# Optimization experiments

Measured on AMD Instinct MI355X. Metric: run time of the kernel, lower is better.

The kernel has to match this reference:

```python
import jax, jax.numpy as jnp
import numpy as np

EPS = 1e-8  # EPSILON in original repo (sharpen denom); cosine eps matches torch default 1e-8
MAX_SHIFT = 1
M_FEAT = 128


def _lstm_cell(x, h, c, W_ih, W_hh, b_ih, b_hh):
    gates = x @ W_ih.T + b_ih + h @ W_hh.T + b_hh
    i, f, g, o = jnp.split(gates, 4, axis=1)
    c_new = jax.nn.sigmoid(f) * c + jax.nn.sigmoid(i) * jnp.tanh(g)
    h_new = jax.nn.sigmoid(o) * jnp.tanh(c_new)
    return h_new, c_new


def _content_address(bank, k, b):
    # torch cosine_similarity over dim 2: dot / max(|m||k|, eps)
    dot = jnp.einsum('bnm,bm->bn', bank, k)
    denom = jnp.maximum(jnp.linalg.norm(bank, axis=2) * jnp.linalg.norm(k, axis=1, keepdims=True), 1e-8)
    return jax.nn.softmax(b * dot / denom, axis=1)


def _shift(w, s):
    # circular unroll then valid cross-correlation with per-batch kernel s [B, 2*MAX_SHIFT+1]
    wp = jnp.concatenate([w[:, -MAX_SHIFT:], w, w[:, :MAX_SHIFT]], axis=1)
    N = w.shape[1]
    taps = 2 * MAX_SHIFT + 1
    return sum(s[:, i:i + 1] * wp[:, i:i + N] for i in range(taps))


def _sharpen(w, r):
    wr = w ** r
    return wr / (wr.sum(axis=1, keepdims=True) + EPS)


def _move(bank, w_prev, k, b, g, s, r):
    w = _content_address(bank, k, b)
    w = w + (1.0 - g) * w_prev  # faithful: w_c is NOT scaled by g in the source
    w = _shift(w, s)
    return _sharpen(w, r)


def _split_read(p):
    M = M_FEAT
    k = p[:, :M]
    b = jax.nn.softplus(p[:, M:M + 1])
    g = jax.nn.sigmoid(p[:, M + 1:M + 2])
    s = jax.nn.softmax(p[:, M + 2:M + 5], axis=1)
    r = 1.0 + jax.nn.softplus(p[:, M + 5:M + 6])
    return k, b, g, s, r


def _split_write(p):
    M = M_FEAT
    k, b, g, s, r = _split_read(p[:, :M + 6])
    e = jax.nn.sigmoid(p[:, M + 6:M + 6 + M])
    a = p[:, M + 6 + M:M + 6 + 2 * M]
    return k, b, g, s, r, e, a


def setup_inputs() -> dict:
    key = jax.random.key(0)
    ks = jax.random.split(key, 16)
    B, E, H, N, M, O = 64, 256, 512, 4096, 128, 256
    rd_out, wr_out = M + 2 * MAX_SHIFT + 4, 3 * M + 2 * MAX_SHIFT + 4
    sc = 0.05
    return {
        'x': jax.random.normal(ks[0], (B, E), jnp.float32),
        'h_prev': jax.random.normal(ks[1], (B, H), jnp.float32),
        'c_prev': jax.random.normal(ks[2], (B, H), jnp.float32),
        'bank': jax.random.normal(ks[3], (B, N, M), jnp.float32) * 0.1,
        'read_w_prev': jnp.zeros((3, B, N), jnp.float32),
        'write_w_prev': jnp.zeros((3, B, N), jnp.float32),
        'W_ih': jax.random.normal(ks[4], (4 * H, E), jnp.float32) * sc,
        'W_hh': jax.random.normal(ks[5], (4 * H, H), jnp.float32) * sc,
        'b_ih': jax.random.normal(ks[6], (4 * H,), jnp.float32) * sc,
        'b_hh': jax.random.normal(ks[7], (4 * H,), jnp.float32) * sc,
        'read_W': jax.random.normal(ks[8], (3, rd_out, H), jnp.float32) * sc,
        'read_b': jax.random.normal(ks[9], (3, rd_out), jnp.float32) * sc,
        'write_W': jax.random.normal(ks[10], (3, wr_out, H), jnp.float32) * sc,
        'write_b': jax.random.normal(ks[11], (3, wr_out), jnp.float32) * sc,
        'out_W': jax.random.normal(ks[12], (O, 3 * M + H), jnp.float32) * sc,
        'out_b': jax.random.normal(ks[13], (O,), jnp.float32) * sc,
    }


def reference(x, h_prev, c_prev, bank, read_w_prev, write_w_prev,
              W_ih, W_hh, b_ih, b_hh, read_W, read_b, write_W, write_b,
              out_W, out_b):
    h, c = _lstm_cell(x, h_prev, c_prev, W_ih, W_hh, b_ih, b_hh)
    reads = []
    for i in range(3):  # head_num=3, structurally distinct params per head
        # write head: update bank
        pw = h @ write_W[i].T + write_b[i]
        k, b, g, s, r, e, a = _split_write(pw)
        ww = _move(bank, write_w_prev[i], k, b, g, s, r)
        bank = bank * (1.0 - ww[:, :, None] * e[:, None, :]) + ww[:, :, None] * a[:, None, :]
        # read head: read from updated bank
        pr = h @ read_W[i].T + read_b[i]
        k, b, g, s, r = _split_read(pr)
        wr = _move(bank, read_w_prev[i], k, b, g, s, r)
        reads.append(jnp.einsum('bn,bnm->bm', wr, bank))
    out = jnp.concatenate(reads + [h], axis=1) @ out_W.T + out_b
    return out
```

## Files before the change

### kernel.cpp

```cpp
#include <hip/hip_runtime.h>
#include <math.h>

namespace {

constexpr int kB = 64;
constexpr int kN = 4096;
constexpr int kM = 128;
constexpr int kH = 512;
constexpr int kE = 256;
constexpr int kO = 256;
constexpr int kGates = 4 * kH;
constexpr int kCatW = 3 * kM + kH;
constexpr int kPRow = 1600;
constexpr int kWN = kB * kN;
constexpr int GRID = 256;
constexpr int TPB = 512;
constexpr float kLog2e = 1.4426950408889634f;

__device__ __forceinline__ float sigm_(float x) { return 1.f / (1.f + expf(-x)); }
__device__ __forceinline__ float softplus_(float x) { return x > 20.f ? x : log1pf(expf(x)); }

struct Args {
  const float *x, *h_prev, *c_prev, *bank, *read_w_prev, *write_w_prev;
  const float *W_ih, *W_hh, *b_ih, *b_hh, *read_W, *read_b, *write_W, *write_b, *out_W, *out_b;
  float *out;
  float *gates0, *gates1, *praw0, *praw1, *cat;
  float *kwb, *krb, *evb, *avb, *scal, *sdot;
  float *wp0, *wp1, *wp2, *wp3, *wp4, *wp5;
  float *mA, *mB;
  unsigned *gcnt;
  unsigned *bcnt;
};

union SMem {
  struct { float At[64 * 20]; float Wt[64 * 65]; } g;
  struct { float hs[256 * 18]; float Wt[64 * 65]; } p;
  struct { float wb[kN]; float red[8]; } a;
  struct { float nred[4][2]; } s;
  struct { float rl[2 * kM]; } r;
};

__device__ __forceinline__ void barrier_on(unsigned* c, unsigned target) {
  __syncthreads();
  if (threadIdx.x == 0) {
    __builtin_amdgcn_fence(__ATOMIC_RELEASE, "agent");
    __hip_atomic_fetch_add(c, 1u, __ATOMIC_RELAXED, __HIP_MEMORY_SCOPE_AGENT);
    while (__hip_atomic_load(c, __ATOMIC_RELAXED, __HIP_MEMORY_SCOPE_AGENT) < target)
      __builtin_amdgcn_s_sleep(1);
    __builtin_amdgcn_fence(__ATOMIC_ACQUIRE, "agent");
  }
  __syncthreads();
}

__device__ void addr_core8(int tid, float* loc, const float* sc, const float* __restrict__ wp,
                           float* wb, float* red) {
  const float g = sc[1], r = sc[2];
  const float s0 = sc[3], s1c = sc[4], s2 = sc[5];
  const int lane = tid & 63, wid = tid >> 6;
  __syncthreads();
  float mx = loc[0];
#pragma unroll
  for (int i = 1; i < 8; i++) mx = fmaxf(mx, loc[i]);
#pragma unroll
  for (int m = 1; m < 64; m <<= 1) mx = fmaxf(mx, __shfl_xor(mx, m, 64));
  if (lane == 0) red[wid] = mx;
  __syncthreads();
  mx = red[0];
#pragma unroll
  for (int k = 1; k < 8; k++) mx = fmaxf(mx, red[k]);
  float sum = 0.f;
#pragma unroll
  for (int i = 0; i < 8; i++) { loc[i] = exp2f((loc[i] - mx) * kLog2e); sum += loc[i]; }
#pragma unroll
  for (int m = 1; m < 64; m <<= 1) sum += __shfl_xor(sum, m, 64);
  __syncthreads();
  if (lane == 0) red[wid] = sum;
  __syncthreads();
  sum = red[0];
#pragma unroll
  for (int k = 1; k < 8; k++) sum += red[k];
  const float inv = 1.f / sum;
  const float omg = 1.f - g;
#pragma unroll
  for (int i = 0; i < 8; i++) {
    int n = tid + i * TPB;
    wb[n] = loc[i] * inv + omg * wp[n];
  }
  __syncthreads();
  float ssum = 0.f;
#pragma unroll
  for (int i = 0; i < 8; i++) {
    int n = tid + i * TPB;
    float sh = s0 * wb[(n + kN - 1) & (kN - 1)] + s1c * wb[n] + s2 * wb[(n + 1) & (kN - 1)];
    float y = (sh > 0.f) ? exp2f(r * log2f(sh)) : 0.f;
    loc[i] = y;
    ssum += y;
  }
#pragma unroll
  for (int m = 1; m < 64; m <<= 1) ssum += __shfl_xor(ssum, m, 64);
  __syncthreads();
  if (lane == 0) red[wid] = ssum;
  __syncthreads();
  ssum = red[0];
#pragma unroll
  for (int k = 1; k < 8; k++) ssum += red[k];
  const float invs = 1.f / (ssum + 1e-8f);
#pragma unroll
  for (int i = 0; i < 8; i++) loc[i] *= invs;
  __syncthreads();
}

__global__ __launch_bounds__(TPB, 2) void mega(Args P) {
  const int bid = blockIdx.x;
  const int tid = threadIdx.x;
  __shared__ SMem sm;

  const int bb_ = bid & 63;
  const int sub_ = bid >> 6;
  unsigned* bc = P.bcnt + bb_ * 32;

  {
    const int khalf = bid >> 7;
    const int unit = bid & 127;
    const int b0 = (unit >> 5) * 16;
    const int j0 = (unit & 31) * 64;
    const int jg = tid & 63;
    const int bq2 = (tid >> 6) * 2;
    float acc0 = 0.f, acc1 = 0.f;
    for (int kc6 = 0; kc6 < 6; kc6++) {
      const int kc = khalf * 6 + kc6;
      const bool isx = kc < 4;
      const float* A = isx ? P.x : P.h_prev;
      const float* W = isx ? P.W_ih : P.W_hh;
      const int lda = isx ? kE : kH;
      const int k0 = (isx ? kc : (kc - 4)) * 64;
      __syncthreads();
      {
        int bb = tid >> 5;
        int kk = (tid & 31) * 2;
        float2 v = *(const float2*)(A + (size_t)(b0 + bb) * lda + k0 + kk);
        sm.g.At[(kk + 0) * 20 + bb] = v.x;
        sm.g.At[(kk + 1) * 20 + bb] = v.y;
      }
#pragma unroll
      for (int i = 0; i < 2; i++) {
        int idx = tid + i * 512;
        int jj = idx >> 4;
        int kk = (idx & 15) * 4;
        float4 w = *(const float4*)(W + (size_t)(j0 + jj) * lda + k0 + kk);
        sm.g.Wt[(kk + 0) * 65 + jj] = w.x; sm.g.Wt[(kk + 1) * 65 + jj] = w.y;
        sm.g.Wt[(kk + 2) * 65 + jj] = w.z; sm.g.Wt[(kk + 3) * 65 + jj] = w.w;
      }
      __syncthreads();
#pragma unroll 4
      for (int k = 0; k < 64; k++) {
        float2 av = *(const float2*)&sm.g.At[k * 20 + bq2];
        float wv = sm.g.Wt[k * 65 + jg];
        acc0 += av.x * wv; acc1 += av.y * wv;
      }
    }
    float* gd = khalf ? P.gates1 : P.gates0;
    gd[(size_t)(b0 + bq2 + 0) * kGates + j0 + jg] = acc0;
    gd[(size_t)(b0 + bq2 + 1) * kGates + j0 + jg] = acc1;
  }
  barrier_on(P.gcnt, GRID * 1);

  if (bid < 200) {
    const int kh = bid / 100;
    const int u = bid % 100;
    const int b0 = (u / 25) * 16;
    const int jt = u % 25;
    const int j0 = jt * 64;
    const int kbase = kh * 256;
    for (int i = tid; i < 16 * 256; i += TPB) {
      int bb = i >> 8, kl = i & 255;
      int kk = kbase + kl;
      int b = b0 + bb;
      const float* g0 = P.gates0 + (size_t)b * kGates;
      const float* g1 = P.gates1 + (size_t)b * kGates;
      float i_ = g0[kk]        + g1[kk]        + P.b_ih[kk]        + P.b_hh[kk];
      float f_ = g0[512 + kk]  + g1[512 + kk]  + P.b_ih[512 + kk]  + P.b_hh[512 + kk];
      float gg = g0[1024 + kk] + g1[1024 + kk] + P.b_ih[1024 + kk] + P.b_hh[1024 + kk];
      float o_ = g0[1536 + kk] + g1[1536 + kk] + P.b_ih[1536 + kk] + P.b_hh[1536 + kk];
      float c = sigm_(f_) * P.c_prev[(size_t)b * kH + kk] + sigm_(i_) * tanhf(gg);
      float h = sigm_(o_) * tanhf(c);
      sm.p.hs[kl * 18 + bb] = h;
      if (jt == 0) P.cat[(size_t)b * kCatW + 3 * kM + kk] = h;
    }
    const int jg = tid & 63;
    const int bq2 = (tid >> 6) * 2;
    float acc0 = 0.f, acc1 = 0.f;
    for (int kc = 0; kc < 4; kc++) {
      const int k0 = kbase + kc * 64;
      const int kl0 = kc * 64;
      __syncthreads();
#pragma unroll
      for (int i = 0; i < 2; i++) {
        int idx = tid + i * 512;
        int jj = idx >> 4;
        int kk = (idx & 15) * 4;
        int j = j0 + jj;
        float4 w = make_float4(0.f, 0.f, 0.f, 0.f);
        if (j < 1170)      w = *(const float4*)(P.write_W + (size_t)j * kH + k0 + kk);
        else if (j < 1572) w = *(const float4*)(P.read_W + (size_t)(j - 1170) * kH + k0 + kk);
        sm.p.Wt[(kk + 0) * 65 + jj] = w.x; sm.p.Wt[(kk + 1) * 65 + jj] = w.y;
        sm.p.Wt[(kk + 2) * 65 + jj] = w.z; sm.p.Wt[(kk + 3) * 65 + jj] = w.w;
      }
      __syncthreads();
#pragma unroll 4
      for (int k = 0; k < 64; k++) {
        float2 av = *(const float2*)&sm.p.hs[(kl0 + k) * 18 + bq2];
        float wv = sm.p.Wt[k * 65 + jg];
        acc0 += av.x * wv; acc1 += av.y * wv;
      }
    }
    float* pd = kh ? P.praw1 : P.praw0;
    if (j0 + jg < 1572) {
      pd[(size_t)(b0 + bq2 + 0) * kPRow + j0 + jg] = acc0;
      pd[(size_t)(b0 + bq2 + 1) * kPRow + j0 + jg] = acc1;
    }
  }
  barrier_on(P.gcnt, GRID * 2);

  const int b = bb_;
  const size_t brow = (size_t)b * kN;

  if (sub_ == 0) {
    const int m = tid & 127;
    const int hg = tid >> 7;
    const float* pr0 = P.praw0 + (size_t)b * kPRow;
    const float* pr1 = P.praw1 + (size_t)b * kPRow;
    if (tid < 384) P.cat[(size_t)b * kCatW + tid] = 0.f;
    {
      const bool isw = hg < 3;
      const int base = isw ? hg * 390 : 1170;
      const float* bias = isw ? (P.write_b + hg * 390) : P.read_b;
      const int slot = isw ? hg : 3;
      float kv = pr0[base + m] + pr1[base + m] + bias[m];
      if (isw) {
        P.kwb[((size_t)hg * kB + b) * kM + m] = kv;
        P.evb[((size_t)hg * kB + b) * kM + m] =
            sigm_(pr0[base + 134 + m] + pr1[base + 134 + m] + bias[134 + m]);
        P.avb[((size_t)hg * kB + b) * kM + m] =
            pr0[base + 262 + m] + pr1[base + 262 + m] + bias[262 + m];
      } else {
        P.krb[((size_t)0 * kB + b) * kM + m] = kv;
      }
      float sq = kv * kv;
#pragma unroll
      for (int mm = 1; mm < 64; mm <<= 1) sq += __shfl_xor(sq, mm, 64);
      if ((tid & 63) == 0) sm.s.nred[hg][m >> 6] = sq;
      __syncthreads();
      if (m == 0) {
        float* s = P.scal + ((size_t)slot * kB + b) * 8;
        s[0] = softplus_(pr0[base + 128] + pr1[base + 128] + bias[128]);
        s[1] = sigm_(pr0[base + 129] + pr1[base + 129] + bias[129]);
        s[2] = 1.f + softplus_(pr0[base + 133] + pr1[base + 133] + bias[133]);
        float x0 = pr0[base + 130] + pr1[base + 130] + bias[130];
        float x1 = pr0[base + 131] + pr1[base + 131] + bias[131];
        float x2 = pr0[base + 132] + pr1[base + 132] + bias[132];
        float mx = fmaxf(x0, fmaxf(x1, x2));
        float e0 = expf(x0 - mx), e1 = expf(x1 - mx), e2 = expf(x2 - mx);
        float si = 1.f / (e0 + e1 + e2);
        s[3] = e0 * si; s[4] = e1 * si; s[5] = e2 * si;
        s[6] = sqrtf(sm.s.nred[hg][0] + sm.s.nred[hg][1]);
      }
      __syncthreads();
    }
    {
      const int j = (hg < 2) ? hg + 1 : 2;
      const bool act = hg < 2;
      const int base = 1170 + j * 134;
      const float* bias = P.read_b + j * 134;
      const int slot = 3 + j;
      float kv = pr0[base + m] + pr1[base + m] + bias[m];
      if (act) P.krb[((size_t)j * kB + b) * kM + m] = kv;
      float sq = kv * kv;
#pragma unroll
      for (int mm = 1; mm < 64; mm <<= 1) sq += __shfl_xor(sq, mm, 64);
      if ((tid & 63) == 0) sm.s.nred[hg][m >> 6] = sq;
      __syncthreads();
      if (m == 0 && act) {
        float* s = P.scal + ((size_t)slot * kB + b) * 8;
        s[0] = softplus_(pr0[base + 128] + pr1[base + 128] + bias[128]);
        s[1] = sigm_(pr0[base + 129] + pr1[base + 129] + bias[129]);
        s[2] = 1.f + softplus_(pr0[base + 133] + pr1[base + 133] + bias[133]);
        float x0 = pr0[base + 130] + pr1[base + 130] + bias[130];
        float x1 = pr0[base + 131] + pr1[base + 131] + bias[131];
        float x2 = pr0[base + 132] + pr1[base + 132] + bias[132];
        float mx = fmaxf(x0, fmaxf(x1, x2));
        float e0 = expf(x0 - mx), e1 = expf(x1 - mx), e2 = expf(x2 - mx);
        float si = 1.f / (e0 + e1 + e2);
        s[3] = e0 * si; s[4] = e1 * si; s[5] = e2 * si;
        s[6] = sqrtf(sm.s.nred[hg][0] + sm.s.nred[hg][1]);
      }
      __syncthreads();
    }
    if (tid < 64) {
      const float* a0v = P.avb + ((size_t)0 * kB + b) * kM;
      const float* a2v = P.avb + ((size_t)2 * kB + b) * kM;
      const float* u[5] = {a0v, a0v, a0v, a2v, a2v};
      const float* v[5] = {P.krb + ((size_t)0 * kB + b) * kM,
                           P.kwb + ((size_t)1 * kB + b) * kM,
                           a0v,
                           P.krb + ((size_t)2 * kB + b) * kM,
                           a2v};
#pragma unroll
      for (int d = 0; d < 5; d++) {
        float s = u[d][tid] * v[d][tid] + u[d][tid + 64] * v[d][tid + 64];
#pragma unroll
        for (int mm = 1; mm < 64; mm <<= 1) s += __shfl_xor(s, mm, 64);
        if (tid == 0) P.sdot[b * 8 + d] = s;
      }
    }
  }
  barrier_on(bc, 4);

  {
    const int chunk = sub_;
    const int lane = tid & 63, wv = tid >> 6, sub = lane >> 4, lm = lane & 15;
    const int m8 = lm * 8;
    float kw0r[8], kr0r[8], kw1r[8], a0r[8], e0r[8];
#pragma unroll
    for (int t = 0; t < 8; t++) {
      kw0r[t] = P.kwb[((size_t)0 * kB + b) * kM + m8 + t];
      kr0r[t] = P.krb[((size_t)0 * kB + b) * kM + m8 + t];
      kw1r[t] = P.kwb[((size_t)1 * kB + b) * kM + m8 + t];
      a0r[t]  = P.avb[((size_t)0 * kB + b) * kM + m8 + t];
      e0r[t]  = P.evb[((size_t)0 * kB + b) * kM + m8 + t];
    }
    const size_t bbase = (size_t)b * kN * kM;
    const int row0 = chunk * 1024 + wv * 4 + sub;
    const float* base = P.bank + bbase + (size_t)row0 * kM + m8;
    float4 pA0 = *(const float4*)(base);
    float4 pA1 = *(const float4*)(base + 4);
    float4 pB0 = *(const float4*)(base + (size_t)32 * kM);
    float4 pB1 = *(const float4*)(base + (size_t)32 * kM + 4);
    for (int it = 0; it < 32; it++) {
      float v[8];
      if ((it & 1) == 0) {
        v[0]=pA0.x; v[1]=pA0.y; v[2]=pA0.z; v[3]=pA0.w; v[4]=pA1.x; v[5]=pA1.y; v[6]=pA1.z; v[7]=pA1.w;
        if (it + 2 < 32) {
          const float* np = base + (size_t)(it + 2) * 32 * kM;
          pA0 = *(const float4*)np; pA1 = *(const float4*)(np + 4);
        }
      } else {
        v[0]=pB0.x; v[1]=pB0.y; v[2]=pB0.z; v[3]=pB0.w; v[4]=pB1.x; v[5]=pB1.y; v[6]=pB1.z; v[7]=pB1.w;
        if (it + 2 < 32) {
          const float* np = base + (size_t)(it + 2) * 32 * kM;
          pB0 = *(const float4*)np; pB1 = *(const float4*)(np + 4);
        }
      }
      const int row = row0 + it * 32;
      float s[10] = {};
#pragma unroll
      for (int t = 0; t < 8; t++) {
        float be = v[t] * e0r[t];
        s[0] += v[t] * kw0r[t];
        s[1] += v[t] * v[t];
        s[2] += v[t] * kr0r[t];
        s[3] += be * kr0r[t];
        s[4] += v[t] * kw1r[t];
        s[5] += be * kw1r[t];
        s[6] += be * v[t];
        s[7] += be * be;
        s[8] += v[t] * a0r[t];
        s[9] += be * a0r[t];
      }
#pragma unroll
      for (int m = 1; m < 16; m <<= 1)
#pragma unroll
        for (int k = 0; k < 10; k++) s[k] += __shfl_xor(s[k], m, 64);
      if (lm == 0) {
        float4* dst = (float4*)(P.mA + (size_t)(brow + row) * 12);
        dst[0] = make_float4(s[0], s[1], s[2], s[3]);
        dst[1] = make_float4(s[4], s[5], s[6], s[7]);
        dst[2] = make_float4(s[8], s[9], 0.f, 0.f);
      }
    }
  }
  barrier_on(bc, 8);

  if (sub_ < 2) {
    const int role = sub_;
    float loc[8], w0r[8];
    {
      const float* sc = P.scal + ((size_t)0 * kB + b) * 8;
      const float beta = sc[0], kn = sc[6];
#pragma unroll
      for (int i = 0; i < 8; i++) {
        const float* mp = P.mA + (size_t)(brow + tid + i * TPB) * 12;
        float4 q0 = *(const float4*)mp;
        loc[i] = beta * q0.x / fmaxf(sqrtf(fmaxf(q0.y, 0.f)) * kn, 1e-8f);
      }
      addr_core8(tid, loc, sc, P.write_w_prev + brow, sm.a.wb, sm.a.red);
#pragma unroll
      for (int i = 0; i < 8; i++) {
        w0r[i] = loc[i];
        if (role == 0) P.wp0[brow + tid + i * TPB] = loc[i];
      }
    }
    if (role == 0) {
      const float* sc = P.scal + ((size_t)3 * kB + b) * 8;
      const float beta = sc[0], kn = sc[6];
      const float sa0kr0 = P.sdot[b * 8 + 0], sa0a0 = P.sdot[b * 8 + 2];
#pragma unroll
      for (int i = 0; i < 8; i++) {
        const float* mp = P.mA + (size_t)(brow + tid + i * TPB) * 12;
        float4 q0 = *(const float4*)mp;
        float4 q1 = *(const float4*)(mp + 4);
        float4 q2 = *(const float4*)(mp + 8);
        float w0 = w0r[i], w0q = w0 * w0;
        float q1v = q0.y - 2.f * w0 * q1.z + w0q * q1.w + 2.f * w0 * q2.x
                  - 2.f * w0q * q2.y + w0q * sa0a0;
        float d = q0.z - w0 * q0.w + w0 * sa0kr0;
        loc[i] = beta * d / fmaxf(sqrtf(fmaxf(q1v, 0.f)) * kn, 1e-8f);
      }
      addr_core8(tid, loc, sc, P.read_w_prev + brow, sm.a.wb, sm.a.red);
#pragma unroll
      for (int i = 0; i < 8; i++) P.wp2[brow + tid + i * TPB] = loc[i];
    } else {
      const float* sc = P.scal + ((size_t)1 * kB + b) * 8;
      const float beta = sc[0], kn = sc[6];
      const float sa0kw1 = P.sdot[b * 8 + 1], sa0a0 = P.sdot[b * 8 + 2];
#pragma unroll
      for (int i = 0; i < 8; i++) {
        const float* mp = P.mA + (size_t)(brow + tid + i * TPB) * 12;
        float4 q0 = *(const float4*)mp;
        float4 q1 = *(const float4*)(mp + 4);
        float4 q2 = *(const float4*)(mp + 8);
        float w0 = w0r[i], w0q = w0 * w0;
        float q1v = q0.y - 2.f * w0 * q1.z + w0q * q1.w + 2.f * w0 * q2.x
                  - 2.f * w0q * q2.y + w0q * sa0a0;
        float d = q1.x - w0 * q1.y + w0 * sa0kw1;
        loc[i] = beta * d / fmaxf(sqrtf(fmaxf(q1v, 0.f)) * kn, 1e-8f);
      }
      addr_core8(tid, loc, sc, P.write_w_prev + (size_t)kWN + brow, sm.a.wb, sm.a.red);
#pragma unroll
      for (int i = 0; i < 8; i++) P.wp1[brow + tid + i * TPB] = loc[i];
    }
  }
  barrier_on(bc, 12);

  {
    const int chunk = sub_;
    const int lane = tid & 63, wv = tid >> 6, sub = lane >> 4, lm = lane & 15;
    const int m8 = lm * 8;
    float e0r[8], a0r[8], e1r[8], a1r[8], kr1r[8], kw2r[8], kr2r[8], e2r[8], a2r[8];
#pragma unroll
    for (int t = 0; t < 8; t++) {
      e0r[t]  = P.evb[((size_t)0 * kB + b) * kM + m8 + t];
      a0r[t]  = P.avb[((size_t)0 * kB + b) * kM + m8 + t];
      e1r[t]  = P.evb[((size_t)1 * kB + b) * kM + m8 + t];
      a1r[t]  = P.avb[((size_t)1 * kB + b) * kM + m8 + t];
      kr1r[t] = P.krb[((size_t)1 * kB + b) * kM + m8 + t];
      kw2r[t] = P.kwb[((size_t)2 * kB + b) * kM + m8 + t];
      kr2r[t] = P.krb[((size_t)2 * kB + b) * kM + m8 + t];
      e2r[t]  = P.evb[((size_t)2 * kB + b) * kM + m8 + t];
      a2r[t]  = P.avb[((size_t)2 * kB + b) * kM + m8 + t];
    }
    float racc[8] = {};
    if (tid < kM) sm.r.rl[tid] = 0.f;
    const size_t bbase = (size_t)b * kN * kM;
    const int row0 = chunk * 1024 + wv * 4 + sub;
    const float* base = P.bank + bbase + (size_t)row0 * kM + m8;
    const size_t wrow = brow + row0;
    float4 pA0 = *(const float4*)(base);
    float4 pA1 = *(const float4*)(base + 4);
    float4 pB0 = *(const float4*)(base + (size_t)32 * kM);
    float4 pB1 = *(const float4*)(base + (size_t)32 * kM + 4);
    float w0A = P.wp0[wrow], w1A = P.wp1[wrow], r0A = P.wp2[wrow];
    float w0B = P.wp0[wrow + 32], w1B = P.wp1[wrow + 32], r0B = P.wp2[wrow + 32];
    for (int it = 0; it < 32; it++) {
      float v[8];
      float w0, w1, wr0;
      if ((it & 1) == 0) {
        v[0]=pA0.x; v[1]=pA0.y; v[2]=pA0.z; v[3]=pA0.w; v[4]=pA1.x; v[5]=pA1.y; v[6]=pA1.z; v[7]=pA1.w;
        w0 = w0A; w1 = w1A; wr0 = r0A;
        if (it + 2 < 32) {
          const float* np = base + (size_t)(it + 2) * 32 * kM;
          pA0 = *(const float4*)np; pA1 = *(const float4*)(np + 4);
          size_t wn = wrow + (size_t)(it + 2) * 32;
          w0A = P.wp0[wn]; w1A = P.wp1[wn]; r0A = P.wp2[wn];
        }
      } else {
        v[0]=pB0.x; v[1]=pB0.y; v[2]=pB0.z; v[3]=pB0.w; v[4]=pB1.x; v[5]=pB1.y; v[6]=pB1.z; v[7]=pB1.w;
        w0 = w0B; w1 = w1B; wr0 = r0B;
        if (it + 2 < 32) {
          const float* np = base + (size_t)(it + 2) * 32 * kM;
          pB0 = *(const float4*)np; pB1 = *(const float4*)(np + 4);
          size_t wn = wrow + (size_t)(it + 2) * 32;
          w0B = P.wp0[wn]; w1B = P.wp1[wn]; r0B = P.wp2[wn];
        }
      }
      const int row = row0 + it * 32;
#pragma unroll
      for (int t = 0; t < 8; t++) {
        v[t] += w0 * (a0r[t] - e0r[t] * v[t]);
        racc[t] += wr0 * v[t];
        v[t] += w1 * (a1r[t] - e1r[t] * v[t]);
      }
      float s[9] = {};
#pragma unroll
      for (int t = 0; t < 8; t++) {
        float ve = v[t] * e2r[t];
        s[0] += v[t] * kr1r[t];
        s[1] += v[t] * kw2r[t];
        s[2] += v[t] * v[t];
        s[3] += v[t] * kr2r[t];
        s[4] += ve * kr2r[t];
        s[5] += ve * v[t];
        s[6] += ve * ve;
        s[7] += v[t] * a2r[t];
        s[8] += ve * a2r[t];
      }
#pragma unroll
      for (int m = 1; m < 16; m <<= 1)
#pragma unroll
        for (int k = 0; k < 9; k++) s[k] += __shfl_xor(s[k], m, 64);
      if (lm == 0) {
        float4* dst = (float4*)(P.mB + (size_t)(brow + row) * 12);
        dst[0] = make_float4(s[0], s[1], s[2], s[3]);
        dst[1] = make_float4(s[4], s[5], s[6], s[7]);
        dst[2] = make_float4(s[8], 0.f, 0.f, 0.f);
      }
    }
    __syncthreads();
#pragma unroll
    for (int t = 0; t < 8; t++) {
      racc[t] += __shfl_xor(racc[t], 16, 64);
      racc[t] += __shfl_xor(racc[t], 32, 64);
    }
    if (sub == 0) {
#pragma unroll
      for (int t = 0; t < 8; t++) atomicAdd(&sm.r.rl[m8 + t], racc[t]);
    }
    __syncthreads();
    if (tid < kM) atomicAdd(&P.cat[(size_t)b * kCatW + tid], sm.r.rl[tid]);
  }
  barrier_on(bc, 16);

  if (sub_ < 2) {
    const int role = sub_;
    float loc[8];
    if (role == 0) {
      float w2r[8];
      {
        const float* sc = P.scal + ((size_t)2 * kB + b) * 8;
        const float beta = sc[0], kn = sc[6];
#pragma unroll
        for (int i = 0; i < 8; i++) {
          const float* mp = P.mB + (size_t)(brow + tid + i * TPB) * 12;
          float4 q0 = *(const float4*)mp;
          loc[i] = beta * q0.y / fmaxf(sqrtf(fmaxf(q0.z, 0.f)) * kn, 1e-8f);
        }
        addr_core8(tid, loc, sc, P.write_w_prev + (size_t)2 * kWN + brow, sm.a.wb, sm.a.red);
#pragma unroll
        for (int i = 0; i < 8; i++) {
          P.wp3[brow + tid + i * TPB] = loc[i];
          w2r[i] = loc[i];
        }
      }
      {
        const float* sc = P.scal + ((size_t)5 * kB + b) * 8;
        const float beta = sc[0], kn = sc[6];
        const float sa2kr2 = P.sdot[b * 8 + 3], sa2a2 = P.sdot[b * 8 + 4];
#pragma unroll
        for (int i = 0; i < 8; i++) {
          const float* mp = P.mB + (size_t)(brow + tid + i * TPB) * 12;
          float4 q0 = *(const float4*)mp;
          float4 q1 = *(const float4*)(mp + 4);
          float4 q2 = *(const float4*)(mp + 8);
          float w2 = w2r[i], w2q = w2 * w2;
          float q3 = q0.z - 2.f * w2 * q1.y + w2q * q1.z + 2.f * w2 * q1.w
                   - 2.f * w2q * q2.x + w2q * sa2a2;
          float d = q0.w - w2 * q1.x + w2 * sa2kr2;
          loc[i] = beta * d / fmaxf(sqrtf(fmaxf(q3, 0.f)) * kn, 1e-8f);
        }
        addr_core8(tid, loc, sc, P.read_w_prev + (size_t)2 * kWN + brow, sm.a.wb, sm.a.red);
#pragma unroll
        for (int i = 0; i < 8; i++) P.wp5[brow + tid + i * TPB] = loc[i];
      }
    } else {
      {
        const float* sc = P.scal + ((size_t)4 * kB + b) * 8;
        const float beta = sc[0], kn = sc[6];
#pragma unroll
        for (int i = 0; i < 8; i++) {
          const float* mp = P.mB + (size_t)(brow + tid + i * TPB) * 12;
          float4 q0 = *(const float4*)mp;
          loc[i] = beta * q0.x / fmaxf(sqrtf(fmaxf(q0.z, 0.f)) * kn, 1e-8f);
        }
        addr_core8(tid, loc, sc, P.read_w_prev + (size_t)kWN + brow, sm.a.wb, sm.a.red);
#pragma unroll
        for (int i = 0; i < 8; i++) P.wp4[brow + tid + i * TPB] = loc[i];
      }
    }
  }
  barrier_on(bc, 20);

  {
    const int chunk = sub_;
    const int lane = tid & 63, wv = tid >> 6, sub = lane >> 4, lm = lane & 15;
    const int m8 = lm * 8;
    float e_r[3][8], a_r[3][8];
#pragma unroll
    for (int j = 0; j < 3; j++)
#pragma unroll
      for (int t = 0; t < 8; t++) {
        e_r[j][t] = P.evb[((size_t)j * kB + b) * kM + m8 + t];
        a_r[j][t] = P.avb[((size_t)j * kB + b) * kM + m8 + t];
      }
    float racc1[8] = {}, racc2[8] = {};
    if (tid < kM) { sm.r.rl[tid] = 0.f; sm.r.rl[kM + tid] = 0.f; }
    const size_t bbase = (size_t)b * kN * kM;
    const int row0 = chunk * 1024 + wv * 4 + sub;
    const float* base = P.bank + bbase + (size_t)row0 * kM + m8;
    const size_t wrow = brow + row0;
    float4 pA0 = *(const float4*)(base);
    float4 pA1 = *(const float4*)(base + 4);
    float4 pB0 = *(const float4*)(base + (size_t)32 * kM);
    float4 pB1 = *(const float4*)(base + (size_t)32 * kM + 4);
    float c0A = P.wp0[wrow], c1A = P.wp1[wrow], c2A = P.wp3[wrow], c3A = P.wp4[wrow], c4A = P.wp5[wrow];
    float c0B = P.wp0[wrow + 32], c1B = P.wp1[wrow + 32], c2B = P.wp3[wrow + 32],
          c3B = P.wp4[wrow + 32], c4B = P.wp5[wrow + 32];
    for (int it = 0; it < 32; it++) {
      float v[8];
      float w0, w1, w2, wr1, wr2;
      if ((it & 1) == 0) {
        v[0]=pA0.x; v[1]=pA0.y; v[2]=pA0.z; v[3]=pA0.w; v[4]=pA1.x; v[5]=pA1.y; v[6]=pA1.z; v[7]=pA1.w;
        w0 = c0A; w1 = c1A; w2 = c2A; wr1 = c3A; wr2 = c4A;
        if (it + 2 < 32) {
          const float* np = base + (size_t)(it + 2) * 32 * kM;
          pA0 = *(const float4*)np; pA1 = *(const float4*)(np + 4);
          size_t wn = wrow + (size_t)(it + 2) * 32;
          c0A = P.wp0[wn]; c1A = P.wp1[wn]; c2A = P.wp3[wn]; c3A = P.wp4[wn]; c4A = P.wp5[wn];
        }
      } else {
        v[0]=pB0.x; v[1]=pB0.y; v[2]=pB0.z; v[3]=pB0.w; v[4]=pB1.x; v[5]=pB1.y; v[6]=pB1.z; v[7]=pB1.w;
        w0 = c0B; w1 = c1B; w2 = c2B; wr1 = c3B; wr2 = c4B;
        if (it + 2 < 32) {
          const float* np = base + (size_t)(it + 2) * 32 * kM;
          pB0 = *(const float4*)np; pB1 = *(const float4*)(np + 4);
          size_t wn = wrow + (size_t)(it + 2) * 32;
          c0B = P.wp0[wn]; c1B = P.wp1[wn]; c2B = P.wp3[wn]; c3B = P.wp4[wn]; c4B = P.wp5[wn];
        }
      }
#pragma unroll
      for (int t = 0; t < 8; t++) {
        v[t] += w0 * (a_r[0][t] - e_r[0][t] * v[t]);
        v[t] += w1 * (a_r[1][t] - e_r[1][t] * v[t]);
        racc1[t] += wr1 * v[t];
        v[t] += w2 * (a_r[2][t] - e_r[2][t] * v[t]);
        racc2[t] += wr2 * v[t];
      }
    }
    __syncthreads();
#pragma unroll
    for (int t = 0; t < 8; t++) {
      racc1[t] += __shfl_xor(racc1[t], 16, 64);
      racc1[t] += __shfl_xor(racc1[t], 32, 64);
      racc2[t] += __shfl_xor(racc2[t], 16, 64);
      racc2[t] += __shfl_xor(racc2[t], 32, 64);
    }
    if (sub == 0) {
#pragma unroll
      for (int t = 0; t < 8; t++) {
        atomicAdd(&sm.r.rl[m8 + t], racc1[t]);
        atomicAdd(&sm.r.rl[kM + m8 + t], racc2[t]);
      }
    }
    __syncthreads();
    if (tid < kM) {
      atomicAdd(&P.cat[(size_t)b * kCatW + kM + tid], sm.r.rl[tid]);
      atomicAdd(&P.cat[(size_t)b * kCatW + 2 * kM + tid], sm.r.rl[kM + tid]);
    }
  }
  barrier_on(bc, 24);

  {
    const int j = sub_ * 64 + (tid >> 3);
    const int ks = (tid & 7) * 112;
    const float* crow = P.cat + (size_t)b * kCatW;
    const float* wrow = P.out_W + (size_t)j * kCatW;
    float acc = 0.f;
#pragma unroll 7
    for (int k = 0; k < 112; k += 4) {
      float4 cv = *(const float4*)(crow + ks + k);
      float4 wv = *(const float4*)(wrow + ks + k);
      acc += cv.x * wv.x + cv.y * wv.y + cv.z * wv.z + cv.w * wv.w;
    }
    acc += __shfl_xor(acc, 1, 64);
    acc += __shfl_xor(acc, 2, 64);
    acc += __shfl_xor(acc, 4, 64);
    if ((tid & 7) == 0) P.out[(size_t)b * kO + j] = P.out_b[j] + acc;
  }
}

}

extern "C" void kernel_launch(void* const* d_in, const int* in_sizes, int n_in,
                              void* d_out, int out_size, void* d_ws, size_t ws_size,
                              hipStream_t stream) {
  Args A_;
  A_.x            = (const float*)d_in[0];
  A_.h_prev       = (const float*)d_in[1];
  A_.c_prev       = (const float*)d_in[2];
  A_.bank         = (const float*)d_in[3];
  A_.read_w_prev  = (const float*)d_in[4];
  A_.write_w_prev = (const float*)d_in[5];
  A_.W_ih         = (const float*)d_in[6];
  A_.W_hh         = (const float*)d_in[7];
  A_.b_ih         = (const float*)d_in[8];
  A_.b_hh         = (const float*)d_in[9];
  A_.read_W       = (const float*)d_in[10];
  A_.read_b       = (const float*)d_in[11];
  A_.write_W      = (const float*)d_in[12];
  A_.write_b      = (const float*)d_in[13];
  A_.out_W        = (const float*)d_in[14];
  A_.out_b        = (const float*)d_in[15];
  A_.out = (float*)d_out;

  float* ws = (float*)d_ws;
  A_.gcnt = (unsigned*)d_ws;
  A_.bcnt = (unsigned*)d_ws + 64;
  float* p = ws + 4096;
  A_.gates0 = p; p += (size_t)kB * kGates;
  A_.gates1 = p; p += (size_t)kB * kGates;
  A_.praw0  = p; p += (size_t)kB * kPRow;
  A_.praw1  = p; p += (size_t)kB * kPRow;
  A_.cat    = p; p += (size_t)kB * kCatW;
  A_.kwb    = p; p += (size_t)3 * kB * kM;
  A_.krb    = p; p += (size_t)3 * kB * kM;
  A_.evb    = p; p += (size_t)3 * kB * kM;
  A_.avb    = p; p += (size_t)3 * kB * kM;
  A_.scal   = p; p += (size_t)6 * kB * 8;
  A_.sdot   = p; p += (size_t)kB * 8;
  A_.wp0    = p; p += (size_t)kWN;
  A_.wp1    = p; p += (size_t)kWN;
  A_.wp2    = p; p += (size_t)kWN;
  A_.wp3    = p; p += (size_t)kWN;
  A_.wp4    = p; p += (size_t)kWN;
  A_.wp5    = p; p += (size_t)kWN;
  A_.mA     = p; p += (size_t)kWN * 12;
  A_.mB     = p; p += (size_t)kWN * 12;

  hipMemsetAsync(d_ws, 0, 16384, stream);
  mega<<<dim3(GRID), dim3(TPB), 0, stream>>>(A_);

  (void)in_sizes; (void)n_in; (void)out_size; (void)ws_size;
}
```

Before: 430.8 us.

## Double persistent grid to 512 blocks, splitting each batch's work across eight blocks

Raises the persistent grid from 256 to 512 blocks and the launch-bounds occupancy target from 2 to 4 blocks per CU. The LSTM gate GEMM is split four ways over K into four partial buffers. The projection GEMM uses 8-row batch tiles. Each bank sweep now covers 512 rows per block instead of 1024, and the output GEMM uses 16-way K splits. The per-batch barrier counts are doubled to match. The aim is more concurrent memory traffic over the large bank, at the cost of more barrier participants, extra partial-sum traffic, and tighter register limits that could cause spills.

```diff
diff --git a/kernel.cpp b/kernel.cpp
--- a/kernel.cpp
+++ b/kernel.cpp
@@ -13,7 +13,7 @@
 constexpr int kCatW = 3 * kM + kH;
 constexpr int kPRow = 1600;
 constexpr int kWN = kB * kN;
-constexpr int GRID = 256;
+constexpr int GRID = 512;
 constexpr int TPB = 512;
 constexpr float kLog2e = 1.4426950408889634f;
 
@@ -24,7 +24,7 @@
   const float *x, *h_prev, *c_prev, *bank, *read_w_prev, *write_w_prev;
   const float *W_ih, *W_hh, *b_ih, *b_hh, *read_W, *read_b, *write_W, *write_b, *out_W, *out_b;
   float *out;
-  float *gates0, *gates1, *praw0, *praw1, *cat;
+  float *gates0, *gates1, *gates2, *gates3, *praw0, *praw1, *cat;
   float *kwb, *krb, *evb, *avb, *scal, *sdot;
   float *wp0, *wp1, *wp2, *wp3, *wp4, *wp5;
   float *mA, *mB;
@@ -34,7 +34,7 @@
 
 union SMem {
   struct { float At[64 * 20]; float Wt[64 * 65]; } g;
-  struct { float hs[256 * 18]; float Wt[64 * 65]; } p;
+  struct { float hs[256 * 10]; float Wt[64 * 65]; } p;
   struct { float wb[kN]; float red[8]; } a;
   struct { float nred[4][2]; } s;
   struct { float rl[2 * kM]; } r;
@@ -110,7 +110,7 @@
   __syncthreads();
 }
 
-__global__ __launch_bounds__(TPB, 2) void mega(Args P) {
+__global__ __launch_bounds__(TPB, 4) void mega(Args P) {
   const int bid = blockIdx.x;
   const int tid = threadIdx.x;
   __shared__ SMem sm;
@@ -120,15 +120,15 @@
   unsigned* bc = P.bcnt + bb_ * 32;
 
   {
-    const int khalf = bid >> 7;
+    const int quarter = bid >> 7;
     const int unit = bid & 127;
     const int b0 = (unit >> 5) * 16;
     const int j0 = (unit & 31) * 64;
     const int jg = tid & 63;
     const int bq2 = (tid >> 6) * 2;
     float acc0 = 0.f, acc1 = 0.f;
-    for (int kc6 = 0; kc6 < 6; kc6++) {
-      const int kc = khalf * 6 + kc6;
+    for (int kc3 = 0; kc3 < 3; kc3++) {
+      const int kc = quarter * 3 + kc3;
       const bool isx = kc < 4;
       const float* A = isx ? P.x : P.h_prev;
       const float* W = isx ? P.W_ih : P.W_hh;
@@ -159,37 +159,40 @@
         acc0 += av.x * wv; acc1 += av.y * wv;
       }
     }
-    float* gd = khalf ? P.gates1 : P.gates0;
+    float* gd = quarter == 0 ? P.gates0 : quarter == 1 ? P.gates1
+              : quarter == 2 ? P.gates2 : P.gates3;
     gd[(size_t)(b0 + bq2 + 0) * kGates + j0 + jg] = acc0;
     gd[(size_t)(b0 + bq2 + 1) * kGates + j0 + jg] = acc1;
   }
   barrier_on(P.gcnt, GRID * 1);
 
-  if (bid < 200) {
-    const int kh = bid / 100;
-    const int u = bid % 100;
-    const int b0 = (u / 25) * 16;
+  if (bid < 400) {
+    const int kh = bid / 200;
+    const int u = bid % 200;
+    const int b0 = (u / 25) * 8;
     const int jt = u % 25;
     const int j0 = jt * 64;
     const int kbase = kh * 256;
-    for (int i = tid; i < 16 * 256; i += TPB) {
+    for (int i = tid; i < 8 * 256; i += TPB) {
       int bb = i >> 8, kl = i & 255;
       int kk = kbase + kl;
       int b = b0 + bb;
       const float* g0 = P.gates0 + (size_t)b * kGates;
       const float* g1 = P.gates1 + (size_t)b * kGates;
-      float i_ = g0[kk]        + g1[kk]        + P.b_ih[kk]        + P.b_hh[kk];
-      float f_ = g0[512 + kk]  + g1[512 + kk]  + P.b_ih[512 + kk]  + P.b_hh[512 + kk];
-      float gg = g0[1024 + kk] + g1[1024 + kk] + P.b_ih[1024 + kk] + P.b_hh[1024 + kk];
-      float o_ = g0[1536 + kk] + g1[1536 + kk] + P.b_ih[1536 + kk] + P.b_hh[1536 + kk];
+      const float* g2 = P.gates2 + (size_t)b * kGates;
+      const float* g3 = P.gates3 + (size_t)b * kGates;
+      float i_ = g0[kk]        + g1[kk]        + g2[kk]        + g3[kk]        + P.b_ih[kk]        + P.b_hh[kk];
+      float f_ = g0[512 + kk]  + g1[512 + kk]  + g2[512 + kk]  + g3[512 + kk]  + P.b_ih[512 + kk]  + P.b_hh[512 + kk];
+      float gg = g0[1024 + kk] + g1[1024 + kk] + g2[1024 + kk] + g3[1024 + kk] + P.b_ih[1024 + kk] + P.b_hh[1024 + kk];
+      float o_ = g0[1536 + kk] + g1[1536 + kk] + g2[1536 + kk] + g3[1536 + kk] + P.b_ih[1536 + kk] + P.b_hh[1536 + kk];
       float c = sigm_(f_) * P.c_prev[(size_t)b * kH + kk] + sigm_(i_) * tanhf(gg);
       float h = sigm_(o_) * tanhf(c);
-      sm.p.hs[kl * 18 + bb] = h;
+      sm.p.hs[kl * 10 + bb] = h;
       if (jt == 0) P.cat[(size_t)b * kCatW + 3 * kM + kk] = h;
     }
     const int jg = tid & 63;
-    const int bq2 = (tid >> 6) * 2;
-    float acc0 = 0.f, acc1 = 0.f;
+    const int bq = tid >> 6;
+    float acc = 0.f;
     for (int kc = 0; kc < 4; kc++) {
       const int k0 = kbase + kc * 64;
       const int kl0 = kc * 64;
@@ -208,17 +211,11 @@
       }
       __syncthreads();
 #pragma unroll 4
-      for (int k = 0; k < 64; k++) {
-        float2 av = *(const float2*)&sm.p.hs[(kl0 + k) * 18 + bq2];
-        float wv = sm.p.Wt[k * 65 + jg];
-        acc0 += av.x * wv; acc1 += av.y * wv;
-      }
+      for (int k = 0; k < 64; k++)
+        acc += sm.p.hs[(kl0 + k) * 10 + bq] * sm.p.Wt[k * 65 + jg];
     }
     float* pd = kh ? P.praw1 : P.praw0;
-    if (j0 + jg < 1572) {
-      pd[(size_t)(b0 + bq2 + 0) * kPRow + j0 + jg] = acc0;
-      pd[(size_t)(b0 + bq2 + 1) * kPRow + j0 + jg] = acc1;
-    }
+    if (j0 + jg < 1572) pd[(size_t)(b0 + bq) * kPRow + j0 + jg] = acc;
   }
   barrier_on(P.gcnt, GRID * 2);
 
@@ -314,7 +311,7 @@
       }
     }
   }
-  barrier_on(bc, 4);
+  barrier_on(bc, 8);
 
   {
     const int chunk = sub_;
@@ -330,23 +327,23 @@
       e0r[t]  = P.evb[((size_t)0 * kB + b) * kM + m8 + t];
     }
     const size_t bbase = (size_t)b * kN * kM;
-    const int row0 = chunk * 1024 + wv * 4 + sub;
+    const int row0 = chunk * 512 + wv * 4 + sub;
     const float* base = P.bank + bbase + (size_t)row0 * kM + m8;
     float4 pA0 = *(const float4*)(base);
     float4 pA1 = *(const float4*)(base + 4);
     float4 pB0 = *(const float4*)(base + (size_t)32 * kM);
     float4 pB1 = *(const float4*)(base + (size_t)32 * kM + 4);
-    for (int it = 0; it < 32; it++) {
+    for (int it = 0; it < 16; it++) {
       float v[8];
       if ((it & 1) == 0) {
         v[0]=pA0.x; v[1]=pA0.y; v[2]=pA0.z; v[3]=pA0.w; v[4]=pA1.x; v[5]=pA1.y; v[6]=pA1.z; v[7]=pA1.w;
-        if (it + 2 < 32) {
+        if (it + 2 < 16) {
           const float* np = base + (size_t)(it + 2) * 32 * kM;
           pA0 = *(const float4*)np; pA1 = *(const float4*)(np + 4);
         }
       } else {
         v[0]=pB0.x; v[1]=pB0.y; v[2]=pB0.z; v[3]=pB0.w; v[4]=pB1.x; v[5]=pB1.y; v[6]=pB1.z; v[7]=pB1.w;
-        if (it + 2 < 32) {
+        if (it + 2 < 16) {
           const float* np = base + (size_t)(it + 2) * 32 * kM;
           pB0 = *(const float4*)np; pB1 = *(const float4*)(np + 4);
         }
@@ -379,7 +376,7 @@
       }
     }
   }
-  barrier_on(bc, 8);
+  barrier_on(bc, 16);
 
   if (sub_ < 2) {
     const int role = sub_;
@@ -440,7 +437,7 @@
       for (int i = 0; i < 8; i++) P.wp1[brow + tid + i * TPB] = loc[i];
     }
   }
-  barrier_on(bc, 12);
+  barrier_on(bc, 24);
 
   {
     const int chunk = sub_;
@@ -462,7 +459,7 @@
     float racc[8] = {};
     if (tid < kM) sm.r.rl[tid] = 0.f;
     const size_t bbase = (size_t)b * kN * kM;
-    const int row0 = chunk * 1024 + wv * 4 + sub;
+    const int row0 = chunk * 512 + wv * 4 + sub;
     const float* base = P.bank + bbase + (size_t)row0 * kM + m8;
     const size_t wrow = brow + row0;
     float4 pA0 = *(const float4*)(base);
@@ -471,13 +468,13 @@
     float4 pB1 = *(const float4*)(base + (size_t)32 * kM + 4);
     float w0A = P.wp0[wrow], w1A = P.wp1[wrow], r0A = P.wp2[wrow];
     float w0B = P.wp0[wrow + 32], w1B = P.wp1[wrow + 32], r0B = P.wp2[wrow + 32];
-    for (int it = 0; it < 32; it++) {
+    for (int it = 0; it < 16; it++) {
       float v[8];
       float w0, w1, wr0;
       if ((it & 1) == 0) {
         v[0]=pA0.x; v[1]=pA0.y; v[2]=pA0.z; v[3]=pA0.w; v[4]=pA1.x; v[5]=pA1.y; v[6]=pA1.z; v[7]=pA1.w;
         w0 = w0A; w1 = w1A; wr0 = r0A;
-        if (it + 2 < 32) {
+        if (it + 2 < 16) {
           const float* np = base + (size_t)(it + 2) * 32 * kM;
           pA0 = *(const float4*)np; pA1 = *(const float4*)(np + 4);
           size_t wn = wrow + (size_t)(it + 2) * 32;
@@ -486,7 +483,7 @@
       } else {
         v[0]=pB0.x; v[1]=pB0.y; v[2]=pB0.z; v[3]=pB0.w; v[4]=pB1.x; v[5]=pB1.y; v[6]=pB1.z; v[7]=pB1.w;
         w0 = w0B; w1 = w1B; wr0 = r0B;
-        if (it + 2 < 32) {
+        if (it + 2 < 16) {
           const float* np = base + (size_t)(it + 2) * 32 * kM;
           pB0 = *(const float4*)np; pB1 = *(const float4*)(np + 4);
           size_t wn = wrow + (size_t)(it + 2) * 32;
@@ -538,7 +535,7 @@
     __syncthreads();
     if (tid < kM) atomicAdd(&P.cat[(size_t)b * kCatW + tid], sm.r.rl[tid]);
   }
-  barrier_on(bc, 16);
+  barrier_on(bc, 32);
 
   if (sub_ < 2) {
     const int role = sub_;
@@ -597,7 +594,7 @@
       }
     }
   }
-  barrier_on(bc, 20);
+  barrier_on(bc, 40);
 
   {
     const int chunk = sub_;
@@ -614,7 +611,7 @@
     float racc1[8] = {}, racc2[8] = {};
     if (tid < kM) { sm.r.rl[tid] = 0.f; sm.r.rl[kM + tid] = 0.f; }
     const size_t bbase = (size_t)b * kN * kM;
-    const int row0 = chunk * 1024 + wv * 4 + sub;
+    const int row0 = chunk * 512 + wv * 4 + sub;
     const float* base = P.bank + bbase + (size_t)row0 * kM + m8;
     const size_t wrow = brow + row0;
     float4 pA0 = *(const float4*)(base);
@@ -624,13 +621,13 @@
     float c0A = P.wp0[wrow], c1A = P.wp1[wrow], c2A = P.wp3[wrow], c3A = P.wp4[wrow], c4A = P.wp5[wrow];
     float c0B = P.wp0[wrow + 32], c1B = P.wp1[wrow + 32], c2B = P.wp3[wrow + 32],
           c3B = P.wp4[wrow + 32], c4B = P.wp5[wrow + 32];
-    for (int it = 0; it < 32; it++) {
+    for (int it = 0; it < 16; it++) {
       float v[8];
       float w0, w1, w2, wr1, wr2;
       if ((it & 1) == 0) {
         v[0]=pA0.x; v[1]=pA0.y; v[2]=pA0.z; v[3]=pA0.w; v[4]=pA1.x; v[5]=pA1.y; v[6]=pA1.z; v[7]=pA1.w;
         w0 = c0A; w1 = c1A; w2 = c2A; wr1 = c3A; wr2 = c4A;
-        if (it + 2 < 32) {
+        if (it + 2 < 16) {
           const float* np = base + (size_t)(it + 2) * 32 * kM;
           pA0 = *(const float4*)np; pA1 = *(const float4*)(np + 4);
           size_t wn = wrow + (size_t)(it + 2) * 32;
@@ -639,7 +636,7 @@
       } else {
         v[0]=pB0.x; v[1]=pB0.y; v[2]=pB0.z; v[3]=pB0.w; v[4]=pB1.x; v[5]=pB1.y; v[6]=pB1.z; v[7]=pB1.w;
         w0 = c0B; w1 = c1B; w2 = c2B; wr1 = c3B; wr2 = c4B;
-        if (it + 2 < 32) {
+        if (it + 2 < 16) {
           const float* np = base + (size_t)(it + 2) * 32 * kM;
           pB0 = *(const float4*)np; pB1 = *(const float4*)(np + 4);
           size_t wn = wrow + (size_t)(it + 2) * 32;
@@ -676,16 +673,16 @@
       atomicAdd(&P.cat[(size_t)b * kCatW + 2 * kM + tid], sm.r.rl[kM + tid]);
     }
   }
-  barrier_on(bc, 24);
+  barrier_on(bc, 48);
 
   {
-    const int j = sub_ * 64 + (tid >> 3);
-    const int ks = (tid & 7) * 112;
+    const int j = sub_ * 32 + (tid >> 4);
+    const int ks = (tid & 15) * 56;
     const float* crow = P.cat + (size_t)b * kCatW;
     const float* wrow = P.out_W + (size_t)j * kCatW;
     float acc = 0.f;
 #pragma unroll 7
-    for (int k = 0; k < 112; k += 4) {
+    for (int k = 0; k < 56; k += 4) {
       float4 cv = *(const float4*)(crow + ks + k);
       float4 wv = *(const float4*)(wrow + ks + k);
       acc += cv.x * wv.x + cv.y * wv.y + cv.z * wv.z + cv.w * wv.w;
@@ -693,7 +690,8 @@
     acc += __shfl_xor(acc, 1, 64);
     acc += __shfl_xor(acc, 2, 64);
     acc += __shfl_xor(acc, 4, 64);
-    if ((tid & 7) == 0) P.out[(size_t)b * kO + j] = P.out_b[j] + acc;
+    acc += __shfl_xor(acc, 8, 64);
+    if ((tid & 15) == 0) P.out[(size_t)b * kO + j] = P.out_b[j] + acc;
   }
 }
 
@@ -727,6 +725,8 @@
   float* p = ws + 4096;
   A_.gates0 = p; p += (size_t)kB * kGates;
   A_.gates1 = p; p += (size_t)kB * kGates;
+  A_.gates2 = p; p += (size_t)kB * kGates;
+  A_.gates3 = p; p += (size_t)kB * kGates;
   A_.praw0  = p; p += (size_t)kB * kPRow;
   A_.praw1  = p; p += (size_t)kB * kPRow;
   A_.cat    = p; p += (size_t)kB * kCatW;
```

Measured after the change: 672.2 us. 1.56x slower.
